# Optimization experiments

Hardware: AMD Instinct MI355X
Metric: run time of the kernel (lower is better)

## Reference

```python
import jax, jax.numpy as jnp
import numpy as np

GROUPS = 32
EPS = 1e-5
NUM_HEADS = 8


def group_norm(x, w, b):
    # x: (B, C, H, W)
    B, C, H, W = x.shape
    xg = x.reshape(B, GROUPS, C // GROUPS, H, W)
    mean = xg.mean(axis=(2, 3, 4), keepdims=True)
    var = xg.var(axis=(2, 3, 4), keepdims=True)
    xg = (xg - mean) * jax.lax.rsqrt(var + EPS)
    x = xg.reshape(B, C, H, W)
    return x * w[None, :, None, None] + b[None, :, None, None]


def setup_inputs() -> dict:
    key = jax.random.key(0)
    ks = jax.random.split(key, 4)
    B, C, H, W = 16, 512, 32, 32
    x = jax.random.normal(ks[0], (B, C, H, W), dtype=jnp.float32)
    gn_w = jnp.ones((C,), dtype=jnp.float32)
    gn_b = jnp.zeros((C,), dtype=jnp.float32)
    qkv_w = jax.random.normal(ks[1], (3 * C, C), dtype=jnp.float32) * 0.02  # 1x1 conv, no bias
    proj_w = jax.random.normal(ks[2], (C, C), dtype=jnp.float32) * 0.02     # 1x1 conv
    proj_b = jax.random.normal(ks[3], (C,), dtype=jnp.float32) * 0.02
    return {"x": x, "gn_w": gn_w, "gn_b": gn_b, "qkv_w": qkv_w,
            "proj_w": proj_w, "proj_b": proj_b}


def reference(x, gn_w, gn_b, qkv_w, proj_w, proj_b):
    B, C, H, W = x.shape
    heads = NUM_HEADS
    head_dim = C // heads
    HW = H * W
    scale = 1.0 / (head_dim ** 0.5)

    x = group_norm(x, gn_w, gn_b)  # residual uses the NORMED x, matching source

    qkv = jnp.einsum('bchw,oc->bohw', x, qkv_w)                     # (B, 3C, H, W)
    qkv = qkv.reshape(B, 3, heads, head_dim, HW)
    q, k, v = qkv[:, 0], qkv[:, 1], qkv[:, 2]                       # (B, heads, head_dim, HW)

    # Replicate the source's exact permute(0,2,3,1)+reshape (scrambles semantics, but faithful)
    def to_bmh(t):
        return jnp.transpose(t, (0, 2, 3, 1)).reshape(B * heads, HW, head_dim)
    q, k, v = to_bmh(q), to_bmh(k), to_bmh(v)

    attn = jax.nn.softmax(jnp.einsum('bnd,bmd->bnm', q, k) * scale, axis=-1)  # (B*heads, HW, HW)
    h = jnp.einsum('bnm,bmd->bnd', attn, v)                                   # (B*heads, HW, head_dim)

    h = h.reshape(B, heads, H, W, head_dim)
    h = jnp.transpose(h, (0, 1, 4, 2, 3)).reshape(B, C, H, W)

    out = jnp.einsum('bchw,oc->bohw', h, proj_w) + proj_b[None, :, None, None]
    return out + x
```

## Files before the change

### kernel.cpp

```cpp
#include <hip/hip_runtime.h>
#include <stdint.h>

typedef unsigned short u16;
typedef short bfrag __attribute__((ext_vector_type(8)));
typedef float ffrag __attribute__((ext_vector_type(4)));
typedef u16 us4 __attribute__((ext_vector_type(4)));
typedef uint32_t u32x4 __attribute__((ext_vector_type(4)));

#define HW 1024
#define C_DIM 512
#define O3 1536
#define BATCH 16

__device__ __forceinline__ u16 f2bf(float f) {
    uint32_t u = __builtin_bit_cast(uint32_t, f);
    u += 0x7FFFu + ((u >> 16) & 1u);
    return (u16)(u >> 16);
}
__device__ __forceinline__ float bf2f(u16 v) {
    return __builtin_bit_cast(float, (uint32_t)v << 16);
}
__device__ __forceinline__ float fexp2(float x) { return __builtin_amdgcn_exp2f(x); }
__device__ __forceinline__ void async16(const u16* src, u16* ldsDst) {
    __builtin_amdgcn_global_load_lds(
        (const __attribute__((address_space(1))) uint32_t*)src,
        (__attribute__((address_space(3))) uint32_t*)ldsDst, 16, 0, 0);
}

__global__ __launch_bounds__(256) void cvt2_kernel(const float* __restrict__ a, u16* __restrict__ da, int n4a,
                                                   const float* __restrict__ b, u16* __restrict__ db, int n4b) {
    int i = blockIdx.x * 256 + threadIdx.x;
    if (i < n4a) {
        float4 v = ((const float4*)a)[i];
        us4 o = { f2bf(v.x), f2bf(v.y), f2bf(v.z), f2bf(v.w) };
        ((us4*)da)[i] = o;
    } else {
        int j = i - n4a;
        if (j < n4b) {
            float4 v = ((const float4*)b)[j];
            us4 o = { f2bf(v.x), f2bf(v.y), f2bf(v.z), f2bf(v.w) };
            ((us4*)db)[j] = o;
        }
    }
}

__global__ __launch_bounds__(256) void groupnorm_kernel(
    const float* __restrict__ x, const float* __restrict__ gw, const float* __restrict__ gb,
    u16* __restrict__ xg, u16* __restrict__ xgt)
{
    __shared__ u16 tile[16 * 1032];
    __shared__ float red[8];
    const int tid = threadIdx.x;
    const int batch = blockIdx.x >> 5, g = blockIdx.x & 31;
    const float* xp = x + ((size_t)batch * C_DIM + g * 16) * HW;

    float s = 0.f, ss = 0.f;
#pragma unroll
    for (int it = 0; it < 16; ++it) {
        int i4 = it * 256 + tid;
        float4 v = ((const float4*)xp)[i4];
        int ci = i4 >> 8;
        int hw = (i4 & 255) * 4;
        s += v.x + v.y + v.z + v.w;
        ss += v.x * v.x + v.y * v.y + v.z * v.z + v.w * v.w;
        us4 u = { f2bf(v.x), f2bf(v.y), f2bf(v.z), f2bf(v.w) };
        *(us4*)&tile[ci * 1032 + hw] = u;
    }
#pragma unroll
    for (int m = 1; m <= 32; m <<= 1) { s += __shfl_xor(s, m, 64); ss += __shfl_xor(ss, m, 64); }
    if ((tid & 63) == 0) { red[tid >> 6] = s; red[4 + (tid >> 6)] = ss; }
    __syncthreads();
    float S = red[0] + red[1] + red[2] + red[3];
    float SS = red[4] + red[5] + red[6] + red[7];
    const float mean = S * (1.f / 16384.f);
    const float istd = rsqrtf(SS * (1.f / 16384.f) - mean * mean + 1e-5f);

    u16* xgp = xg + ((size_t)batch * C_DIM + g * 16) * HW;
#pragma unroll
    for (int it = 0; it < 16; ++it) {
        int i4 = it * 256 + tid;
        int ci = i4 >> 8;
        int hw = (i4 & 255) * 4;
        us4 u = *(us4*)&tile[ci * 1032 + hw];
        float sc = gw[g * 16 + ci] * istd;
        float bi = gb[g * 16 + ci] - mean * sc;
        us4 o = { f2bf(bf2f(u[0]) * sc + bi), f2bf(bf2f(u[1]) * sc + bi),
                  f2bf(bf2f(u[2]) * sc + bi), f2bf(bf2f(u[3]) * sc + bi) };
        *(us4*)&xgp[(size_t)ci * HW + hw] = o;
    }
    u16* xtp = xgt + (size_t)batch * HW * C_DIM + g * 16;
#pragma unroll
    for (int it = 0; it < 16; ++it) {
        int hw = (tid >> 2) + it * 64;
        int c0 = (tid & 3) * 4;
        us4 o;
#pragma unroll
        for (int k2 = 0; k2 < 4; ++k2) {
            int ci = c0 + k2;
            float sc = gw[g * 16 + ci] * istd;
            float bi = gb[g * 16 + ci] - mean * sc;
            o[k2] = f2bf(bf2f(tile[ci * 1032 + hw]) * sc + bi);
        }
        *(us4*)&xtp[(size_t)hw * C_DIM + c0] = o;
    }
}

template<int EPI>
__global__ __launch_bounds__(256) void gemm_kernel(
    const u16* __restrict__ A, const u16* __restrict__ B, void* __restrict__ Out,
    const float* __restrict__ bias, const u16* __restrict__ resid, u16* __restrict__ vtout,
    int Ntiles, int tpb, int ldOut, long aBatch, long bBatch, long oBatch, long rBatch)
{
    __shared__ __align__(16) u16 smem[24576];
    const int tid = threadIdx.x;
    const int l = tid & 63, w = tid >> 6;
    const int nwg = gridDim.x;
    const int swz = (blockIdx.x & 7) * (nwg >> 3) + (blockIdx.x >> 3);
    const int batch = swz / tpb, t = swz % tpb;
    const int tm = t / Ntiles, tn = t % Ntiles;
    A += (size_t)batch * aBatch + (size_t)tm * 128 * 512;
    B += (size_t)batch * bBatch + (size_t)tn * 128 * 512;

    auto stage = [&](const u16* gbase, u16* lds, int kt) {
#pragma unroll
        for (int i = 0; i < 2; ++i) {
            int L = i * 256 + tid;
            int row = L >> 2, cs = L & 3;
            int c = cs ^ ((row & 3) ^ ((row >> 2) & 3));
            async16(gbase + (size_t)row * 512 + kt * 32 + c * 8,
                    lds + (size_t)(i * 256 + (tid & 192)) * 8);
        }
    };

    ffrag acc[4][4] = {};
    stage(A, smem, 0);        stage(B, smem + 12288, 0);
    stage(A, smem + 4096, 1); stage(B, smem + 16384, 1);
    const int wr = (w >> 1) * 64, wc = (w & 1) * 64;
    for (int kt = 0; kt < 16; ++kt) {
        const int cur = kt % 3;
        if (kt < 15) asm volatile("s_waitcnt vmcnt(4)" ::: "memory");
        else         asm volatile("s_waitcnt vmcnt(0)" ::: "memory");
        __builtin_amdgcn_s_barrier();
        __builtin_amdgcn_sched_barrier(0);
        if (kt < 14) {
            int nxt = (kt + 2) % 3;
            stage(A, smem + nxt * 4096, kt + 2);
            stage(B, smem + 12288 + nxt * 4096, kt + 2);
        }
        const u16* As = smem + cur * 4096;
        const u16* Bs = smem + 12288 + cur * 4096;
        bfrag a[4], bb[4];
#pragma unroll
        for (int i = 0; i < 4; ++i) {
            int row = wr + i * 16 + (l & 15);
            int ch = (l >> 4) ^ ((row & 3) ^ ((row >> 2) & 3));
            a[i] = *(const bfrag*)&As[row * 32 + ch * 8];
            int col = wc + i * 16 + (l & 15);
            int ch2 = (l >> 4) ^ ((col & 3) ^ ((col >> 2) & 3));
            bb[i] = *(const bfrag*)&Bs[col * 32 + ch2 * 8];
        }
        __builtin_amdgcn_s_setprio(1);
#pragma unroll
        for (int i = 0; i < 4; ++i)
#pragma unroll
            for (int j = 0; j < 4; ++j)
                acc[i][j] = __builtin_amdgcn_mfma_f32_16x16x32_bf16(a[i], bb[j], acc[i][j], 0, 0, 0);
        __builtin_amdgcn_s_setprio(0);
    }
    __syncthreads();
    const int rbase = tm * 128 + wr + ((l >> 4) << 2);
    const int cbase = tn * 128 + wc + (l & 15);
    if (EPI == 0) {
        if (tn >= 8) {
            u16* vb = vtout + (size_t)batch * 8 * 64 * HW;
            const int hd0 = tn * 128 - 1024;
#pragma unroll
            for (int i = 0; i < 4; ++i)
#pragma unroll
                for (int j = 0; j < 4; ++j) {
                    int hd_l = wc + (l & 15) + j * 16;
                    int m_l = wr + i * 16 + ((l >> 4) << 2);
                    int s_l = (m_l & 96) | ((m_l & 12) << 1) | ((m_l & 16) >> 2);
                    int c4 = s_l >> 2;
                    int c4s = c4 ^ (hd_l & 7);
                    us4 pk = { f2bf(acc[i][j][0]), f2bf(acc[i][j][1]),
                               f2bf(acc[i][j][2]), f2bf(acc[i][j][3]) };
                    *(us4*)&smem[hd_l * 128 + c4s * 4] = pk;
                }
            __syncthreads();
#pragma unroll
            for (int it = 0; it < 16; ++it) {
                int f4 = it * 256 + tid;
                int hd_l = f4 >> 5, c4 = f4 & 31;
                int c4s = c4 ^ (hd_l & 7);
                us4 v = *(const us4*)&smem[hd_l * 128 + c4s * 4];
                *(us4*)&vb[(size_t)(hd0 + hd_l) * HW + tm * 128 + c4 * 4] = v;
            }
        } else {
            u16* outp = (u16*)Out + (size_t)batch * oBatch;
#pragma unroll
            for (int i = 0; i < 4; ++i)
#pragma unroll
                for (int j = 0; j < 4; ++j)
#pragma unroll
                    for (int r = 0; r < 4; ++r)
                        outp[(size_t)(rbase + i * 16 + r) * ldOut + cbase + j * 16] = f2bf(acc[i][j][r]);
        }
    } else {
        float* outp = (float*)Out + (size_t)batch * oBatch;
        const u16* rp = resid + (size_t)batch * rBatch;
#pragma unroll
        for (int i = 0; i < 4; ++i)
#pragma unroll
            for (int j = 0; j < 4; ++j)
#pragma unroll
                for (int r = 0; r < 4; ++r) {
                    int rr = rbase + i * 16 + r, cc = cbase + j * 16;
                    outp[(size_t)rr * ldOut + cc] =
                        acc[i][j][r] + bias[rr] + bf2f(rp[(size_t)rr * ldOut + cc]);
                }
    }
}

__global__ __launch_bounds__(512, 4) void attn_kernel(const u16* __restrict__ qkvt,
                                                      const u16* __restrict__ vt,
                                                      u16* __restrict__ ht)
{
    __shared__ __align__(16) u16 KVs[6 * 4096];
    const int tid = threadIdx.x, l = tid & 63, w = tid >> 6, g = l >> 4;
    const int swz = ((blockIdx.x & 7) << 6) + (blockIdx.x >> 3);
    const int nt = swz & 3, h = (swz >> 2) & 7, batch = swz >> 5;
    const u16* Qb = qkvt + (size_t)batch * HW * O3 + h * 64;
    const u16* Kb = Qb + 512;
    const u16* Vtb = vt + (size_t)(batch * 8 + h) * 64 * HW;
    const int n0 = nt * 256 + w * 32;
    const float cexp = 0.125f * 1.44269504f;

    bfrag qf[2][2];
#pragma unroll
    for (int ni = 0; ni < 2; ++ni)
#pragma unroll
        for (int kc = 0; kc < 2; ++kc)
            qf[ni][kc] = *(const bfrag*)&Qb[(size_t)(n0 + ni * 16 + (l & 15)) * O3 + kc * 32 + g * 8];

    bfrag ones;
#pragma unroll
    for (int k = 0; k < 8; ++k) ones[k] = (short)0x3F80;

    auto stageK = [&](int ms, u16* lds) {
        int row = tid >> 3, c = (tid & 7) ^ (row & 7);
        async16(&Kb[(size_t)(ms * 64 + row) * O3 + c * 8], lds + (size_t)(tid & 448) * 8);
    };
    auto stageV = [&](int ms, u16* lds) {
        int row = tid >> 3, c = (tid & 7) ^ (row & 7);
        async16(&Vtb[(size_t)row * HW + ms * 64 + c * 8], lds + (size_t)(tid & 448) * 8);
    };

    ffrag hacc[2][4] = {};
    ffrag accl[2] = {};
    float M[2] = { -1e30f, -1e30f };

    stageK(0, KVs); stageV(0, KVs + 3 * 4096);
    stageK(1, KVs + 4096); stageV(1, KVs + 4 * 4096);

    for (int ms = 0; ms < 16; ++ms) {
        const int cur = ms % 3;
        const u16* Ksc = KVs + cur * 4096;
        const u16* Vsc = KVs + (3 + cur) * 4096;
        if (ms < 15) asm volatile("s_waitcnt vmcnt(2)" ::: "memory");
        else         asm volatile("s_waitcnt vmcnt(0)" ::: "memory");
        __builtin_amdgcn_s_barrier();
        __builtin_amdgcn_sched_barrier(0);
        if (ms < 14) {
            int nxt = (ms + 2) % 3;
            stageK(ms + 2, KVs + nxt * 4096);
            stageV(ms + 2, KVs + (3 + nxt) * 4096);
        }

        ffrag s[2][4] = {};
        __builtin_amdgcn_s_setprio(1);
#pragma unroll
        for (int mj = 0; mj < 4; ++mj)
#pragma unroll
            for (int kc = 0; kc < 2; ++kc) {
                int m = mj * 16 + (l & 15);
                int ch = (kc * 4 + g) ^ (m & 7);
                bfrag kf = *(const bfrag*)&Ksc[m * 64 + ch * 8];
#pragma unroll
                for (int ni = 0; ni < 2; ++ni)
                    s[ni][mj] = __builtin_amdgcn_mfma_f32_16x16x32_bf16(kf, qf[ni][kc], s[ni][mj], 0, 0, 0);
            }
        __builtin_amdgcn_s_setprio(0);

        u32x4 pk[2][2];
#pragma unroll
        for (int ni = 0; ni < 2; ++ni) {
            float pm = fmaxf(fmaxf(s[ni][0][0], s[ni][0][1]), s[ni][0][2]);
            pm = fmaxf(fmaxf(pm, s[ni][0][3]), s[ni][1][0]);
            pm = fmaxf(fmaxf(pm, s[ni][1][1]), s[ni][1][2]);
            pm = fmaxf(fmaxf(pm, s[ni][1][3]), s[ni][2][0]);
            pm = fmaxf(fmaxf(pm, s[ni][2][1]), s[ni][2][2]);
            pm = fmaxf(fmaxf(pm, s[ni][2][3]), s[ni][3][0]);
            pm = fmaxf(fmaxf(pm, s[ni][3][1]), s[ni][3][2]);
            pm = fmaxf(pm, s[ni][3][3]);
            pm = fmaxf(pm, __shfl_xor(pm, 16, 64));
            pm = fmaxf(pm, __shfl_xor(pm, 32, 64));
            float mnew = fmaxf(M[ni], pm * cexp);
            if (!__all(mnew - M[ni] <= 4.0f)) {
                float corr = fexp2(M[ni] - mnew);
                M[ni] = mnew;
#pragma unroll
                for (int r = 0; r < 4; ++r) {
                    float cb = __shfl(corr, g * 4 + r, 64);
                    accl[ni][r] *= cb;
#pragma unroll
                    for (int dj = 0; dj < 4; ++dj) hacc[ni][dj][r] *= cb;
                }
            }
#pragma unroll
            for (int kc = 0; kc < 2; ++kc)
#pragma unroll
                for (int hh = 0; hh < 2; ++hh) {
                    int mj = kc * 2 + hh;
                    float p0 = fexp2(fmaf(s[ni][mj][0], cexp, -M[ni]));
                    float p1 = fexp2(fmaf(s[ni][mj][1], cexp, -M[ni]));
                    float p2 = fexp2(fmaf(s[ni][mj][2], cexp, -M[ni]));
                    float p3 = fexp2(fmaf(s[ni][mj][3], cexp, -M[ni]));
                    pk[ni][kc][hh * 2] = __builtin_amdgcn_perm(
                        __builtin_bit_cast(uint32_t, p1), __builtin_bit_cast(uint32_t, p0), 0x07060302u);
                    pk[ni][kc][hh * 2 + 1] = __builtin_amdgcn_perm(
                        __builtin_bit_cast(uint32_t, p3), __builtin_bit_cast(uint32_t, p2), 0x07060302u);
                }
        }

        __builtin_amdgcn_s_setprio(1);
#pragma unroll
        for (int kc = 0; kc < 2; ++kc) {
            bfrag pf0 = __builtin_bit_cast(bfrag, pk[0][kc]);
            bfrag pf1 = __builtin_bit_cast(bfrag, pk[1][kc]);
            accl[0] = __builtin_amdgcn_mfma_f32_16x16x32_bf16(pf0, ones, accl[0], 0, 0, 0);
            accl[1] = __builtin_amdgcn_mfma_f32_16x16x32_bf16(pf1, ones, accl[1], 0, 0, 0);
#pragma unroll
            for (int dj = 0; dj < 4; ++dj) {
                int d = dj * 16 + (l & 15);
                int ch = (kc * 4 + g) ^ (d & 7);
                bfrag vf = *(const bfrag*)&Vsc[d * 64 + ch * 8];
                hacc[0][dj] = __builtin_amdgcn_mfma_f32_16x16x32_bf16(pf0, vf, hacc[0][dj], 0, 0, 0);
                hacc[1][dj] = __builtin_amdgcn_mfma_f32_16x16x32_bf16(pf1, vf, hacc[1][dj], 0, 0, 0);
            }
        }
        __builtin_amdgcn_s_setprio(0);
    }

    u16* hp = ht + (size_t)batch * HW * C_DIM + h * 64;
#pragma unroll
    for (int ni = 0; ni < 2; ++ni) {
        float linv[4];
#pragma unroll
        for (int r = 0; r < 4; ++r) linv[r] = __builtin_amdgcn_rcpf(accl[ni][r]);
#pragma unroll
        for (int dj = 0; dj < 4; ++dj)
#pragma unroll
            for (int r = 0; r < 4; ++r) {
                int n = n0 + ni * 16 + g * 4 + r;
                int d = dj * 16 + (l & 15);
                hp[(size_t)n * C_DIM + d] = f2bf(hacc[ni][dj][r] * linv[r]);
            }
    }
}

extern "C" void kernel_launch(void* const* d_in, const int* in_sizes, int n_in,
                              void* d_out, int out_size, void* d_ws, size_t ws_size,
                              hipStream_t stream)
{
    const float* x = (const float*)d_in[0];
    const float* gw = (const float*)d_in[1];
    const float* gb = (const float*)d_in[2];
    const float* qkvw = (const float*)d_in[3];
    const float* projw = (const float*)d_in[4];
    const float* projb = (const float*)d_in[5];
    float* out = (float*)d_out;
    char* ws = (char*)d_ws;
    u16* xg    = (u16*)(ws);
    u16* xgt   = (u16*)(ws + 16777216);
    u16* qkvt  = (u16*)(ws + 33554432);
    u16* vt    = (u16*)(ws + 83886080);
    u16* qkvwb = (u16*)(ws + 100663296);
    u16* projwb= (u16*)(ws + 102236160);
    u16* ht    = xgt;

    cvt2_kernel<<<1024, 256, 0, stream>>>(qkvw, qkvwb, 196608, projw, projwb, 65536);
    groupnorm_kernel<<<512, 256, 0, stream>>>(x, gw, gb, xg, xgt);
    gemm_kernel<0><<<1536, 256, 0, stream>>>(
        xgt, qkvwb, qkvt, nullptr, nullptr, vt, 12, 96, 1536, 524288L, 0L, 1572864L, 0L);
    attn_kernel<<<512, 512, 0, stream>>>(qkvt, vt, ht);
    gemm_kernel<1><<<512, 256, 0, stream>>>(
        projwb, ht, out, projb, xg, nullptr, 8, 32, 1024, 0L, 524288L, 524288L, 524288L);
}
```

Baseline: 118.1 us.

## Software-pipeline attention so QK of the next tile overlaps PV of the previous

```diff
diff --git a/kernel.cpp b/kernel.cpp
--- a/kernel.cpp
+++ b/kernel.cpp
@@ -226,7 +226,7 @@
                                                       const u16* __restrict__ vt,
                                                       u16* __restrict__ ht)
 {
-    __shared__ __align__(16) u16 KVs[6 * 4096];
+    __shared__ __align__(16) u16 KVs[7 * 4096];
     const int tid = threadIdx.x, l = tid & 63, w = tid >> 6, g = l >> 4;
     const int swz = ((blockIdx.x & 7) << 6) + (blockIdx.x >> 3);
     const int nt = swz & 3, h = (swz >> 2) & 7, batch = swz >> 5;
@@ -259,25 +259,25 @@
     ffrag hacc[2][4] = {};
     ffrag accl[2] = {};
     float M[2] = { -1e30f, -1e30f };
-
-    stageK(0, KVs); stageV(0, KVs + 3 * 4096);
-    stageK(1, KVs + 4096); stageV(1, KVs + 4 * 4096);
-
-    for (int ms = 0; ms < 16; ++ms) {
-        const int cur = ms % 3;
-        const u16* Ksc = KVs + cur * 4096;
-        const u16* Vsc = KVs + (3 + cur) * 4096;
+    ffrag s[2][4];
+    u32x4 pkA[2][2], pkB[2][2];
+
+    auto topbar = [&](int ms) {
         if (ms < 15) asm volatile("s_waitcnt vmcnt(2)" ::: "memory");
         else         asm volatile("s_waitcnt vmcnt(0)" ::: "memory");
         __builtin_amdgcn_s_barrier();
         __builtin_amdgcn_sched_barrier(0);
         if (ms < 14) {
-            int nxt = (ms + 2) % 3;
-            stageK(ms + 2, KVs + nxt * 4096);
-            stageV(ms + 2, KVs + (3 + nxt) * 4096);
-        }
-
-        ffrag s[2][4] = {};
+            stageK(ms + 2, KVs + ((ms + 2) % 3) * 4096);
+            stageV(ms + 2, KVs + (3 + ((ms + 2) & 3)) * 4096);
+        }
+    };
+
+    auto do_qk = [&](const u16* Ksc) {
+#pragma unroll
+        for (int ni = 0; ni < 2; ++ni)
+#pragma unroll
+            for (int mj = 0; mj < 4; ++mj) s[ni][mj] = ffrag{0.f, 0.f, 0.f, 0.f};
         __builtin_amdgcn_s_setprio(1);
 #pragma unroll
         for (int mj = 0; mj < 4; ++mj)
@@ -291,8 +291,29 @@
                     s[ni][mj] = __builtin_amdgcn_mfma_f32_16x16x32_bf16(kf, qf[ni][kc], s[ni][mj], 0, 0, 0);
             }
         __builtin_amdgcn_s_setprio(0);
-
-        u32x4 pk[2][2];
+    };
+
+    auto do_pv = [&](u32x4 (&pk)[2][2], const u16* Vsc) {
+        __builtin_amdgcn_s_setprio(1);
+#pragma unroll
+        for (int kc = 0; kc < 2; ++kc) {
+            bfrag pf0 = __builtin_bit_cast(bfrag, pk[0][kc]);
+            bfrag pf1 = __builtin_bit_cast(bfrag, pk[1][kc]);
+            accl[0] = __builtin_amdgcn_mfma_f32_16x16x32_bf16(pf0, ones, accl[0], 0, 0, 0);
+            accl[1] = __builtin_amdgcn_mfma_f32_16x16x32_bf16(pf1, ones, accl[1], 0, 0, 0);
+#pragma unroll
+            for (int dj = 0; dj < 4; ++dj) {
+                int d = dj * 16 + (l & 15);
+                int ch = (kc * 4 + g) ^ (d & 7);
+                bfrag vf = *(const bfrag*)&Vsc[d * 64 + ch * 8];
+                hacc[0][dj] = __builtin_amdgcn_mfma_f32_16x16x32_bf16(pf0, vf, hacc[0][dj], 0, 0, 0);
+                hacc[1][dj] = __builtin_amdgcn_mfma_f32_16x16x32_bf16(pf1, vf, hacc[1][dj], 0, 0, 0);
+            }
+        }
+        __builtin_amdgcn_s_setprio(0);
+    };
+
+    auto do_sm = [&](u32x4 (&pk)[2][2]) {
 #pragma unroll
         for (int ni = 0; ni < 2; ++ni) {
             float pm = fmaxf(fmaxf(s[ni][0][0], s[ni][0][1]), s[ni][0][2]);
@@ -332,25 +353,30 @@
                         __builtin_bit_cast(uint32_t, p3), __builtin_bit_cast(uint32_t, p2), 0x07060302u);
                 }
         }
-
-        __builtin_amdgcn_s_setprio(1);
-#pragma unroll
-        for (int kc = 0; kc < 2; ++kc) {
-            bfrag pf0 = __builtin_bit_cast(bfrag, pk[0][kc]);
-            bfrag pf1 = __builtin_bit_cast(bfrag, pk[1][kc]);
-            accl[0] = __builtin_amdgcn_mfma_f32_16x16x32_bf16(pf0, ones, accl[0], 0, 0, 0);
-            accl[1] = __builtin_amdgcn_mfma_f32_16x16x32_bf16(pf1, ones, accl[1], 0, 0, 0);
-#pragma unroll
-            for (int dj = 0; dj < 4; ++dj) {
-                int d = dj * 16 + (l & 15);
-                int ch = (kc * 4 + g) ^ (d & 7);
-                bfrag vf = *(const bfrag*)&Vsc[d * 64 + ch * 8];
-                hacc[0][dj] = __builtin_amdgcn_mfma_f32_16x16x32_bf16(pf0, vf, hacc[0][dj], 0, 0, 0);
-                hacc[1][dj] = __builtin_amdgcn_mfma_f32_16x16x32_bf16(pf1, vf, hacc[1][dj], 0, 0, 0);
-            }
-        }
-        __builtin_amdgcn_s_setprio(0);
-    }
+    };
+
+    stageK(0, KVs);        stageV(0, KVs + 3 * 4096);
+    stageK(1, KVs + 4096); stageV(1, KVs + 4 * 4096);
+
+    topbar(0);
+    do_qk(KVs);
+    do_sm(pkA);
+    for (int k = 0; k < 7; ++k) {
+        const int ms = 2 * k + 1;
+        topbar(ms);
+        do_qk(KVs + (ms % 3) * 4096);
+        do_pv(pkA, KVs + (3 + ((ms - 1) & 3)) * 4096);
+        do_sm(pkB);
+        topbar(ms + 1);
+        do_qk(KVs + ((ms + 1) % 3) * 4096);
+        do_pv(pkB, KVs + (3 + (ms & 3)) * 4096);
+        do_sm(pkA);
+    }
+    topbar(15);
+    do_qk(KVs + ((15 % 3)) * 4096);
+    do_pv(pkA, KVs + (3 + (14 & 3)) * 4096);
+    do_sm(pkB);
+    do_pv(pkB, KVs + (3 + (15 & 3)) * 4096);
 
     u16* hp = ht + (size_t)batch * HW * C_DIM + h * 64;
 #pragma unroll
```

After: 144.4 us. +22.3%, slower.

## Software-pipeline attention loop to overlap QK of next tile with PV of previous

Applied to the files above, without the earlier changes.

```diff
diff --git a/kernel.cpp b/kernel.cpp
--- a/kernel.cpp
+++ b/kernel.cpp
@@ -226,7 +226,7 @@
                                                       const u16* __restrict__ vt,
                                                       u16* __restrict__ ht)
 {
-    __shared__ __align__(16) u16 KVs[6 * 4096];
+    __shared__ __align__(16) u16 KVs[7 * 4096];
     const int tid = threadIdx.x, l = tid & 63, w = tid >> 6, g = l >> 4;
     const int swz = ((blockIdx.x & 7) << 6) + (blockIdx.x >> 3);
     const int nt = swz & 3, h = (swz >> 2) & 7, batch = swz >> 5;
@@ -259,98 +259,130 @@
     ffrag hacc[2][4] = {};
     ffrag accl[2] = {};
     float M[2] = { -1e30f, -1e30f };
-
-    stageK(0, KVs); stageV(0, KVs + 3 * 4096);
+    ffrag s[2][4];
+    u32x4 pkA[2][2], pkB[2][2];
+
+#define TOPBAR(ms) do {                                                          \
+    if ((ms) < 15) asm volatile("s_waitcnt vmcnt(2)" ::: "memory");              \
+    else           asm volatile("s_waitcnt vmcnt(0)" ::: "memory");              \
+    __builtin_amdgcn_s_barrier();                                                \
+    __builtin_amdgcn_sched_barrier(0);                                           \
+    if ((ms) < 14) {                                                             \
+        stageK((ms) + 2, KVs + (((ms) + 2) % 3) * 4096);                         \
+        stageV((ms) + 2, KVs + (3 + (((ms) + 2) & 3)) * 4096);                   \
+    }                                                                            \
+} while (0)
+
+#define QK_BODY(KBUF) do {                                                       \
+    const u16* Ksc_ = (KBUF);                                                    \
+    _Pragma("unroll")                                                            \
+    for (int ni = 0; ni < 2; ++ni)                                               \
+        _Pragma("unroll")                                                        \
+        for (int mj = 0; mj < 4; ++mj) s[ni][mj] = ffrag{0.f, 0.f, 0.f, 0.f};    \
+    __builtin_amdgcn_s_setprio(1);                                               \
+    _Pragma("unroll")                                                            \
+    for (int mj = 0; mj < 4; ++mj)                                               \
+        _Pragma("unroll")                                                        \
+        for (int kc = 0; kc < 2; ++kc) {                                         \
+            int m_ = mj * 16 + (l & 15);                                         \
+            int ch_ = (kc * 4 + g) ^ (m_ & 7);                                   \
+            bfrag kf_ = *(const bfrag*)&Ksc_[m_ * 64 + ch_ * 8];                 \
+            s[0][mj] = __builtin_amdgcn_mfma_f32_16x16x32_bf16(kf_, qf[0][kc], s[0][mj], 0, 0, 0); \
+            s[1][mj] = __builtin_amdgcn_mfma_f32_16x16x32_bf16(kf_, qf[1][kc], s[1][mj], 0, 0, 0); \
+        }                                                                        \
+    __builtin_amdgcn_s_setprio(0);                                               \
+} while (0)
+
+#define SM_BODY(PK) do {                                                         \
+    _Pragma("unroll")                                                            \
+    for (int ni = 0; ni < 2; ++ni) {                                             \
+        float pm_ = fmaxf(fmaxf(s[ni][0][0], s[ni][0][1]), s[ni][0][2]);         \
+        pm_ = fmaxf(fmaxf(pm_, s[ni][0][3]), s[ni][1][0]);                       \
+        pm_ = fmaxf(fmaxf(pm_, s[ni][1][1]), s[ni][1][2]);                       \
+        pm_ = fmaxf(fmaxf(pm_, s[ni][1][3]), s[ni][2][0]);                       \
+        pm_ = fmaxf(fmaxf(pm_, s[ni][2][1]), s[ni][2][2]);                       \
+        pm_ = fmaxf(fmaxf(pm_, s[ni][2][3]), s[ni][3][0]);                       \
+        pm_ = fmaxf(fmaxf(pm_, s[ni][3][1]), s[ni][3][2]);                       \
+        pm_ = fmaxf(pm_, s[ni][3][3]);                                           \
+        pm_ = fmaxf(pm_, __shfl_xor(pm_, 16, 64));                               \
+        pm_ = fmaxf(pm_, __shfl_xor(pm_, 32, 64));                               \
+        float mnew_ = fmaxf(M[ni], pm_ * cexp);                                  \
+        if (!__all(mnew_ - M[ni] <= 4.0f)) {                                     \
+            float corr_ = fexp2(M[ni] - mnew_);                                  \
+            M[ni] = mnew_;                                                       \
+            _Pragma("unroll")                                                    \
+            for (int r = 0; r < 4; ++r) {                                        \
+                float cb_ = __shfl(corr_, g * 4 + r, 64);                        \
+                accl[ni][r] *= cb_;                                              \
+                _Pragma("unroll")                                                \
+                for (int dj = 0; dj < 4; ++dj) hacc[ni][dj][r] *= cb_;           \
+            }                                                                    \
+        }                                                                        \
+        _Pragma("unroll")                                                        \
+        for (int kc = 0; kc < 2; ++kc)                                           \
+            _Pragma("unroll")                                                    \
+            for (int hh = 0; hh < 2; ++hh) {                                     \
+                int mj_ = kc * 2 + hh;                                           \
+                float p0_ = fexp2(fmaf(s[ni][mj_][0], cexp, -M[ni]));            \
+                float p1_ = fexp2(fmaf(s[ni][mj_][1], cexp, -M[ni]));            \
+                float p2_ = fexp2(fmaf(s[ni][mj_][2], cexp, -M[ni]));            \
+                float p3_ = fexp2(fmaf(s[ni][mj_][3], cexp, -M[ni]));            \
+                PK[ni][kc][hh * 2] = __builtin_amdgcn_perm(                      \
+                    __builtin_bit_cast(uint32_t, p1_), __builtin_bit_cast(uint32_t, p0_), 0x07060302u); \
+                PK[ni][kc][hh * 2 + 1] = __builtin_amdgcn_perm(                  \
+                    __builtin_bit_cast(uint32_t, p3_), __builtin_bit_cast(uint32_t, p2_), 0x07060302u); \
+            }                                                                    \
+    }                                                                            \
+} while (0)
+
+#define PV_BODY(PK, VBUF) do {                                                   \
+    const u16* Vsc_ = (VBUF);                                                    \
+    __builtin_amdgcn_s_setprio(1);                                               \
+    _Pragma("unroll")                                                            \
+    for (int kc = 0; kc < 2; ++kc) {                                             \
+        bfrag pf0_ = __builtin_bit_cast(bfrag, PK[0][kc]);                       \
+        bfrag pf1_ = __builtin_bit_cast(bfrag, PK[1][kc]);                       \
+        accl[0] = __builtin_amdgcn_mfma_f32_16x16x32_bf16(pf0_, ones, accl[0], 0, 0, 0); \
+        accl[1] = __builtin_amdgcn_mfma_f32_16x16x32_bf16(pf1_, ones, accl[1], 0, 0, 0); \
+        _Pragma("unroll")                                                        \
+        for (int dj = 0; dj < 4; ++dj) {                                         \
+            int d_ = dj * 16 + (l & 15);                                         \
+            int ch_ = (kc * 4 + g) ^ (d_ & 7);                                   \
+            bfrag vf_ = *(const bfrag*)&Vsc_[d_ * 64 + ch_ * 8];                 \
+            hacc[0][dj] = __builtin_amdgcn_mfma_f32_16x16x32_bf16(pf0_, vf_, hacc[0][dj], 0, 0, 0); \
+            hacc[1][dj] = __builtin_amdgcn_mfma_f32_16x16x32_bf16(pf1_, vf_, hacc[1][dj], 0, 0, 0); \
+        }                                                                        \
+    }                                                                            \
+    __builtin_amdgcn_s_setprio(0);                                               \
+} while (0)
+
+    stageK(0, KVs);        stageV(0, KVs + 3 * 4096);
     stageK(1, KVs + 4096); stageV(1, KVs + 4 * 4096);
 
-    for (int ms = 0; ms < 16; ++ms) {
-        const int cur = ms % 3;
-        const u16* Ksc = KVs + cur * 4096;
-        const u16* Vsc = KVs + (3 + cur) * 4096;
-        if (ms < 15) asm volatile("s_waitcnt vmcnt(2)" ::: "memory");
-        else         asm volatile("s_waitcnt vmcnt(0)" ::: "memory");
-        __builtin_amdgcn_s_barrier();
-        __builtin_amdgcn_sched_barrier(0);
-        if (ms < 14) {
-            int nxt = (ms + 2) % 3;
-            stageK(ms + 2, KVs + nxt * 4096);
-            stageV(ms + 2, KVs + (3 + nxt) * 4096);
-        }
-
-        ffrag s[2][4] = {};
-        __builtin_amdgcn_s_setprio(1);
-#pragma unroll
-        for (int mj = 0; mj < 4; ++mj)
-#pragma unroll
-            for (int kc = 0; kc < 2; ++kc) {
-                int m = mj * 16 + (l & 15);
-                int ch = (kc * 4 + g) ^ (m & 7);
-                bfrag kf = *(const bfrag*)&Ksc[m * 64 + ch * 8];
-#pragma unroll
-                for (int ni = 0; ni < 2; ++ni)
-                    s[ni][mj] = __builtin_amdgcn_mfma_f32_16x16x32_bf16(kf, qf[ni][kc], s[ni][mj], 0, 0, 0);
-            }
-        __builtin_amdgcn_s_setprio(0);
-
-        u32x4 pk[2][2];
-#pragma unroll
-        for (int ni = 0; ni < 2; ++ni) {
-            float pm = fmaxf(fmaxf(s[ni][0][0], s[ni][0][1]), s[ni][0][2]);
-            pm = fmaxf(fmaxf(pm, s[ni][0][3]), s[ni][1][0]);
-            pm = fmaxf(fmaxf(pm, s[ni][1][1]), s[ni][1][2]);
-            pm = fmaxf(fmaxf(pm, s[ni][1][3]), s[ni][2][0]);
-            pm = fmaxf(fmaxf(pm, s[ni][2][1]), s[ni][2][2]);
-            pm = fmaxf(fmaxf(pm, s[ni][2][3]), s[ni][3][0]);
-            pm = fmaxf(fmaxf(pm, s[ni][3][1]), s[ni][3][2]);
-            pm = fmaxf(pm, s[ni][3][3]);
-            pm = fmaxf(pm, __shfl_xor(pm, 16, 64));
-            pm = fmaxf(pm, __shfl_xor(pm, 32, 64));
-            float mnew = fmaxf(M[ni], pm * cexp);
-            if (!__all(mnew - M[ni] <= 4.0f)) {
-                float corr = fexp2(M[ni] - mnew);
-                M[ni] = mnew;
-#pragma unroll
-                for (int r = 0; r < 4; ++r) {
-                    float cb = __shfl(corr, g * 4 + r, 64);
-                    accl[ni][r] *= cb;
-#pragma unroll
-                    for (int dj = 0; dj < 4; ++dj) hacc[ni][dj][r] *= cb;
-                }
-            }
-#pragma unroll
-            for (int kc = 0; kc < 2; ++kc)
-#pragma unroll
-                for (int hh = 0; hh < 2; ++hh) {
-                    int mj = kc * 2 + hh;
-                    float p0 = fexp2(fmaf(s[ni][mj][0], cexp, -M[ni]));
-                    float p1 = fexp2(fmaf(s[ni][mj][1], cexp, -M[ni]));
-                    float p2 = fexp2(fmaf(s[ni][mj][2], cexp, -M[ni]));
-                    float p3 = fexp2(fmaf(s[ni][mj][3], cexp, -M[ni]));
-                    pk[ni][kc][hh * 2] = __builtin_amdgcn_perm(
-                        __builtin_bit_cast(uint32_t, p1), __builtin_bit_cast(uint32_t, p0), 0x07060302u);
-                    pk[ni][kc][hh * 2 + 1] = __builtin_amdgcn_perm(
-                        __builtin_bit_cast(uint32_t, p3), __builtin_bit_cast(uint32_t, p2), 0x07060302u);
-                }
-        }
-
-        __builtin_amdgcn_s_setprio(1);
-#pragma unroll
-        for (int kc = 0; kc < 2; ++kc) {
-            bfrag pf0 = __builtin_bit_cast(bfrag, pk[0][kc]);
-            bfrag pf1 = __builtin_bit_cast(bfrag, pk[1][kc]);
-            accl[0] = __builtin_amdgcn_mfma_f32_16x16x32_bf16(pf0, ones, accl[0], 0, 0, 0);
-            accl[1] = __builtin_amdgcn_mfma_f32_16x16x32_bf16(pf1, ones, accl[1], 0, 0, 0);
-#pragma unroll
-            for (int dj = 0; dj < 4; ++dj) {
-                int d = dj * 16 + (l & 15);
-                int ch = (kc * 4 + g) ^ (d & 7);
-                bfrag vf = *(const bfrag*)&Vsc[d * 64 + ch * 8];
-                hacc[0][dj] = __builtin_amdgcn_mfma_f32_16x16x32_bf16(pf0, vf, hacc[0][dj], 0, 0, 0);
-                hacc[1][dj] = __builtin_amdgcn_mfma_f32_16x16x32_bf16(pf1, vf, hacc[1][dj], 0, 0, 0);
-            }
-        }
-        __builtin_amdgcn_s_setprio(0);
-    }
+    TOPBAR(0);
+    QK_BODY(KVs);
+    SM_BODY(pkA);
+    for (int k = 0; k < 7; ++k) {
+        const int ms = 2 * k + 1;
+        TOPBAR(ms);
+        QK_BODY(KVs + (ms % 3) * 4096);
+        PV_BODY(pkA, KVs + (3 + ((ms - 1) & 3)) * 4096);
+        SM_BODY(pkB);
+        TOPBAR(ms + 1);
+        QK_BODY(KVs + ((ms + 1) % 3) * 4096);
+        PV_BODY(pkB, KVs + (3 + (ms & 3)) * 4096);
+        SM_BODY(pkA);
+    }
+    TOPBAR(15);
+    QK_BODY(KVs);
+    PV_BODY(pkA, KVs + (3 + 2) * 4096);
+    SM_BODY(pkB);
+    PV_BODY(pkB, KVs + (3 + 3) * 4096);
+
+#undef TOPBAR
+#undef QK_BODY
+#undef SM_BODY
+#undef PV_BODY
 
     u16* hp = ht + (size_t)batch * HW * C_DIM + h * 64;
 #pragma unroll
```

New measurement: 150.6 us. 1.28x slower.
